# Kernel optimization log

Hardware: AMD Instinct MI355X
Metric: run time of the kernel (lower is better)

The kernel has to match this reference:

```python
import jax, jax.numpy as jnp
import numpy as np

TOP_K = 2000
NUM_DETS = 1000
BASE_LAYER_RANGE = (24.0, 48.0, 24.0, 48.0)  # (min_y, max_y, min_x, max_x) from db.configs


def _topk(heat, K):
    # heat: [B, C, H, W] -> topk over flattened C*H*W (CornerNet-style)
    B, C, H, W = heat.shape
    scores, inds = jax.lax.top_k(heat.reshape(B, -1), K)
    clses = inds // (H * W)
    sp_inds = inds % (H * W)            # spatial index into H*W
    ys = (sp_inds // W).astype(heat.dtype)
    xs = (sp_inds % W).astype(heat.dtype)
    return scores, sp_inds, clses, ys, xs


def _transpose_and_gather(feat, ind):
    # feat: [B, C, H, W], ind: [B, K] spatial indices -> [B, K, C]
    B, C, H, W = feat.shape
    feat = feat.transpose(0, 2, 3, 1).reshape(B, H * W, C)
    return feat[jnp.arange(B)[:, None], ind]


def _gather_feat(feat, ind):
    # feat: [B, N, C], ind: [B, K] -> [B, K, C]
    B = feat.shape[0]
    return feat[jnp.arange(B)[:, None], ind]


def _decode_layer(heat, tl_regr, br_regr, H0, W0, layer_idx):
    B, C, H, W = heat.shape
    dt = heat.dtype
    height_scale = 8.0 * H0 / H
    width_scale = 8.0 * W0 / W
    K = min(TOP_K, H * W)
    scores, inds, clses, ys, xs = _topk(heat, K)
    ys = ys.reshape(B, K, 1)
    xs = xs.reshape(B, K, 1)
    tlr = _transpose_and_gather(tl_regr, inds).reshape(B, K, 1, 2)
    brr = _transpose_and_gather(br_regr, inds).reshape(B, K, 1, 2)
    min_y, max_y, min_x, max_x = [v / 8.0 / 2.0 for v in BASE_LAYER_RANGE]
    tl_xs = xs - ((max_x - min_x) * tlr[..., 0] + (max_x + min_x) / 2.0)
    tl_ys = ys - ((max_y - min_y) * tlr[..., 1] + (max_y + min_y) / 2.0)
    br_xs = xs + ((max_x - min_x) * brr[..., 0] + (max_x + min_x) / 2.0)
    br_ys = ys + ((max_y - min_y) * brr[..., 1] + (max_y + min_y) / 2.0)
    bboxes = jnp.stack((tl_xs, tl_ys, br_xs, br_ys), axis=3)  # [B, K, 1, 4]
    sc = scores.reshape(B, K, 1)
    invalid = (br_xs < tl_xs) | (br_ys < tl_ys)
    sc = jnp.where(invalid, jnp.asarray(-1.0, dt), sc)
    sc = sc.reshape(B, -1)
    nd = min(NUM_DETS, sc.shape[1])
    sc, top = jax.lax.top_k(sc, nd)
    sc = sc[:, :, None]
    bboxes = _gather_feat(bboxes.reshape(B, -1, 4), top)
    bboxes = bboxes * jnp.asarray([width_scale, height_scale, width_scale, height_scale], dt)
    # layer_detections: zeros [B, nd, 7]; [:,:,:5] = cat([scores, bboxes]); then row 6 set to i
    det = jnp.concatenate([sc, bboxes, jnp.zeros((B, nd, 2), dt)], axis=2)
    det = det.at[:, 6, :].set(jnp.asarray(float(layer_idx), dt))  # faithful to `[:, 6] = i`
    return det


def setup_inputs() -> dict:
    key = jax.random.key(0)
    ks = jax.random.split(key, 9)
    B, C = 16, 80
    sizes = [(128, 128), (64, 64), (32, 32)]
    inp = {}
    for i, (H, W) in enumerate(sizes):
        inp[f"heat{i}"] = jax.random.uniform(ks[3 * i], (B, C, H, W), dtype=jnp.float32)
        inp[f"tl{i}"] = jax.random.normal(ks[3 * i + 1], (B, 2, H, W), dtype=jnp.float32)
        inp[f"br{i}"] = jax.random.normal(ks[3 * i + 2], (B, 2, H, W), dtype=jnp.float32)
    return inp


def reference(heat0, heat1, heat2, tl0, tl1, tl2, br0, br1, br2):
    heats = [heat0, heat1, heat2]
    tls = [tl0, tl1, tl2]
    brs = [br0, br1, br2]
    _, _, H0, W0 = heats[0].shape
    dets = [_decode_layer(heats[i], tls[i], brs[i], H0, W0, i) for i in range(3)]
    detections = jnp.concatenate(dets, axis=1)  # [B, sum_nd, 7]
    nd = min(NUM_DETS, detections.shape[1])
    _, top = jax.lax.top_k(detections[:, :, 0], nd)
    return _gather_feat(detections, top)
```

## Files before the change

### kernel.cpp

```cpp
#include <hip/hip_runtime.h>


#define NB 1024
#define CAP2 2048
#define CHUNK_H 32768
#define CHUNK_C 16384
#define LCAP 1024

__device__ __forceinline__ unsigned int ord_f32(float f) {
    unsigned int b = __float_as_uint(f);
    return (b & 0x80000000u) ? ~b : (b | 0x80000000u);
}
__device__ __forceinline__ float unord_f32(unsigned int o) {
    unsigned int b = (o & 0x80000000u) ? (o & 0x7fffffffu) : ~o;
    return __uint_as_float(b);
}
__device__ __forceinline__ int bucket_of(float f) {
    int bi = (int)(f * (float)NB);
    bi = bi < 0 ? 0 : (bi > NB - 1 ? NB - 1 : bi);
    return bi;
}

__device__ __forceinline__ int layer_N(int l)  { return (l == 0) ? 1310720 : (l == 1) ? 327680 : 81920; }
__device__ __forceinline__ int hist_nchunks(int l) { return (l == 0) ? 40 : (l == 1) ? 10 : 3; }
__device__ __forceinline__ int hist_base(int l)    { return (l == 0) ? 0 : (l == 1) ? 640 : 800; }

__global__ __launch_bounds__(256) void hist_kernel(
    const float* __restrict__ h0, const float* __restrict__ h1, const float* __restrict__ h2,
    int* __restrict__ ph)
{
    int l = blockIdx.z, b = blockIdx.y, chunk = blockIdx.x;
    int nc = hist_nchunks(l);
    if (chunk >= nc) return;
    int N = layer_N(l);
    int elems = min(CHUNK_H, N - chunk * CHUNK_H);
    const float* heat = (l == 0) ? h0 : (l == 1) ? h1 : h2;
    __shared__ int lh[NB];
    for (int i = threadIdx.x; i < NB; i += 256) lh[i] = 0;
    __syncthreads();
    const float4* p = (const float4*)(heat + (size_t)b * N + (size_t)chunk * CHUNK_H);
    int n4 = elems >> 2;
    for (int i = threadIdx.x; i < n4; i += 256) {
        float4 v = p[i];
        atomicAdd(&lh[bucket_of(v.x)], 1);
        atomicAdd(&lh[bucket_of(v.y)], 1);
        atomicAdd(&lh[bucket_of(v.z)], 1);
        atomicAdd(&lh[bucket_of(v.w)], 1);
    }
    __syncthreads();
    int pidx = hist_base(l) + b * nc + chunk;
    int* dst = ph + (size_t)pidx * NB;
    for (int i = threadIdx.x; i < NB; i += 256) dst[i] = lh[i];
}

__global__ __launch_bounds__(256) void thresh_kernel(const int* __restrict__ ph,
                                                     int* __restrict__ tb,
                                                     int* __restrict__ cnt)
{
    int b = blockIdx.x & 15;
    int l = blockIdx.x >> 4;
    int bl = l * 16 + b;
    if (threadIdx.x < 2) cnt[bl * 2 + threadIdx.x] = 0;
    int K = (l == 2) ? 1024 : 2000;
    int nc = hist_nchunks(l);
    const int* base = ph + (size_t)(hist_base(l) + b * nc) * NB;
    __shared__ int hh[NB];
    __shared__ int seg[256];
    int s4 = 0;
    for (int j = 0; j < 4; j++) {
        int bkt = threadIdx.x * 4 + j;
        int s = 0;
        for (int c = 0; c < nc; c++) s += base[(size_t)c * NB + bkt];
        hh[bkt] = s;
        s4 += s;
    }
    seg[threadIdx.x] = s4;
    __syncthreads();
    if (threadIdx.x == 0) {
        int acc = 0, si;
        for (si = 255; si >= 0; si--) {
            if (acc + seg[si] >= K) break;
            acc += seg[si];
        }
        if (si < 0) si = 0;
        int bidx = si * 4 + 3;
        for (; bidx > si * 4; bidx--) {
            acc += hh[bidx];
            if (acc >= K) break;
        }
        tb[bl] = bidx;
    }
}

__global__ __launch_bounds__(256) void collect_kernel(
    const float* __restrict__ h0, const float* __restrict__ h1, const float* __restrict__ h2,
    const int* __restrict__ tb, int* __restrict__ cnt, unsigned long long* __restrict__ cand)
{
    int l = blockIdx.z, b = blockIdx.y, chunk = blockIdx.x;
    int N = layer_N(l);
    if (chunk * CHUNK_C >= N) return;
    const float* heat = (l == 0) ? h0 : (l == 1) ? h1 : h2;
    int t = tb[l * 16 + b];
    int bl = l * 16 + b;

    __shared__ int lc[2];
    __shared__ int gb[2];
    __shared__ unsigned long long lbuf[2][LCAP];
    if (threadIdx.x < 2) lc[threadIdx.x] = 0;
    __syncthreads();

    const float4* p = (const float4*)(heat + (size_t)b * N + (size_t)chunk * CHUNK_C);
    int base = chunk * CHUNK_C;
    for (int i = threadIdx.x; i < CHUNK_C / 4; i += 256) {
        float4 v = p[i];
        float vs[4] = {v.x, v.y, v.z, v.w};
#pragma unroll
        for (int cc = 0; cc < 4; cc++) {
            int bk = bucket_of(vs[cc]);
            if (bk >= t) {
                int which = (bk > t) ? 0 : 1;
                int pos = atomicAdd(&lc[which], 1);
                if (pos < LCAP) {
                    unsigned int idx = (unsigned int)(base + 4 * i + cc);
                    lbuf[which][pos] = ((unsigned long long)ord_f32(vs[cc]) << 32) | (unsigned int)(~idx);
                }
            }
        }
    }
    __syncthreads();
    if (threadIdx.x < 2) {
        int n = min(lc[threadIdx.x], LCAP);
        gb[threadIdx.x] = atomicAdd(cnt + bl * 2 + threadIdx.x, n);
    }
    __syncthreads();
#pragma unroll
    for (int w = 0; w < 2; w++) {
        int n = min(lc[w], LCAP);
        unsigned long long* cd = cand + ((size_t)bl * 2 + w) * CAP2;
        int g0 = gb[w];
        for (int i = threadIdx.x; i < n; i += 256) {
            int pos = g0 + i;
            if (pos < CAP2) cd[pos] = lbuf[w][i];
        }
    }
}


__device__ __forceinline__ unsigned long long shfl_xor_u64(unsigned long long a, int j) {
    unsigned int lo = (unsigned int)a, hi = (unsigned int)(a >> 32);
    lo = (unsigned int)__shfl_xor((int)lo, j, 64);
    hi = (unsigned int)__shfl_xor((int)hi, j, 64);
    return ((unsigned long long)hi << 32) | lo;
}

template<int K, int J>
struct PhaseH {
    static __device__ __forceinline__ void run(unsigned long long (&v)[8], int base, int lane) {
        constexpr int JR = J >> 6;
#pragma unroll
        for (int r = 0; r < 8; r++) {
            if ((r & JR) == 0) {
                int i = base | (r << 6) | lane;
                unsigned long long a = v[r], bb = v[r | JR];
                bool sw = ((i & K) == 0) ? (a < bb) : (a > bb);
                if (sw) { v[r] = bb; v[r | JR] = a; }
            }
        }
        PhaseH<K, (J >> 1)>::run(v, base, lane);
    }
};

template<int K>
struct PhaseH<K, 32> {
    static __device__ __forceinline__ void run(unsigned long long (&v)[8], int base, int lane) {
#pragma unroll
        for (int js = 32; js >= 1; js >>= 1) {
            if (K > js) {
#pragma unroll
                for (int r = 0; r < 8; r++) {
                    unsigned long long a = v[r];
                    unsigned long long w = shfl_xor_u64(a, js);
                    int i = base | (r << 6) | lane;
                    bool upper = (lane & js) != 0;
                    bool keep_max = (((i & K) == 0) != upper);
                    bool agw = a > w;
                    v[r] = (keep_max == agw) ? a : w;
                }
            }
        }
    }
};

template<int K>
struct StageH {
    static __device__ __forceinline__ void run(unsigned long long (&v)[8], int base, int lane) {
        PhaseH<K, (K > 64 ? (K >> 1) : 32)>::run(v, base, lane);
        StageH<(K << 1)>::run(v, base, lane);
    }
};
template<>
struct StageH<1024> {
    static __device__ __forceinline__ void run(unsigned long long (&)[8], int, int) {}
};

template<int K, int J>
__device__ __forceinline__ void lds_exchange(unsigned long long (&v)[8],
                                             unsigned long long* lds, int base, int lane) {
    __syncthreads();
#pragma unroll
    for (int r = 0; r < 8; r++) lds[base | (r << 6) | lane] = v[r];
    __syncthreads();
#pragma unroll
    for (int r = 0; r < 8; r++) {
        int i = base | (r << 6) | lane;
        unsigned long long w = lds[i ^ J];
        bool upper = (i & J) != 0;
        bool keep_max = (((i & K) == 0) != upper);
        bool agw = v[r] > w;
        v[r] = (keep_max == agw) ? v[r] : w;
    }
}

__global__ __launch_bounds__(256) void sort_kernel(const int* __restrict__ cnt,
                                                   unsigned long long* __restrict__ cand)
{
    int idx = blockIdx.x;
    int n = min(cnt[idx], CAP2);
    unsigned long long* src = cand + (size_t)idx * CAP2;
    __shared__ unsigned long long lds[CAP2];
    int tid = threadIdx.x;
    int lane = tid & 63;
    int base = (tid >> 6) << 9;

    unsigned long long v[8];
#pragma unroll
    for (int r = 0; r < 8; r++) {
        int i = base | (r << 6) | lane;
        v[r] = (i < n) ? src[i] : 0ull;
    }

    StageH<2>::run(v, base, lane);

    lds_exchange<1024, 512>(v, lds, base, lane);
    PhaseH<1024, 256>::run(v, base, lane);

    lds_exchange<2048, 1024>(v, lds, base, lane);
    lds_exchange<2048, 512>(v, lds, base, lane);
    PhaseH<2048, 256>::run(v, base, lane);

#pragma unroll
    for (int r = 0; r < 8; r++) src[base | (r << 6) | lane] = v[r];
}

__global__ __launch_bounds__(1024) void build_kernel(
    const float* __restrict__ t0, const float* __restrict__ t1, const float* __restrict__ t2,
    const float* __restrict__ r0, const float* __restrict__ r1, const float* __restrict__ r2,
    const int* __restrict__ cnt, const unsigned long long* __restrict__ cand,
    float* __restrict__ det)
{
    int l = blockIdx.x >> 4;
    int b = blockIdx.x & 15;
    int bl = l * 16 + b;
    int HW = (l == 0) ? 16384 : (l == 1) ? 4096 : 1024;
    int W  = (l == 0) ? 128 : (l == 1) ? 64 : 32;
    int K  = (l == 2) ? 1024 : 2000;
    float scale = (l == 0) ? 8.f : (l == 1) ? 16.f : 32.f;
    const float* tlp = (l == 0) ? t0 : (l == 1) ? t1 : t2;
    const float* brp = (l == 0) ? r0 : (l == 1) ? r1 : r2;

    int n_hi = min(cnt[bl * 2], CAP2);
    const unsigned long long* hi = cand + (size_t)(bl * 2) * CAP2;
    const unsigned long long* bd = cand + (size_t)(bl * 2 + 1) * CAP2;

    __shared__ int wsum[16];
    int tid = threadIdx.x;
    int lane = tid & 63, wid = tid >> 6;

    float s_[2], bx_[2][4];
    int f_[2];
#pragma unroll
    for (int q = 0; q < 2; q++) {
        int k = 2 * tid + q;
        f_[q] = 0;
        if (k < K) {
            unsigned long long kk = (k < n_hi) ? hi[k] : bd[k - n_hi];
            unsigned int idx = ~(unsigned int)kk;
            float score = unord_f32((unsigned int)(kk >> 32));
            int sp = (int)(idx % (unsigned)HW);
            float xs = (float)(sp % W), ys = (float)(sp / W);
            float tv0 = tlp[((size_t)b * 2 + 0) * HW + sp];
            float tv1 = tlp[((size_t)b * 2 + 1) * HW + sp];
            float bv0 = brp[((size_t)b * 2 + 0) * HW + sp];
            float bv1 = brp[((size_t)b * 2 + 1) * HW + sp];
            float tlx = __fsub_rn(xs, __fadd_rn(__fmul_rn(1.5f, tv0), 2.25f));
            float tly = __fsub_rn(ys, __fadd_rn(__fmul_rn(1.5f, tv1), 2.25f));
            float brx = __fadd_rn(xs, __fadd_rn(__fmul_rn(1.5f, bv0), 2.25f));
            float bry = __fadd_rn(ys, __fadd_rn(__fmul_rn(1.5f, bv1), 2.25f));
            bool invalid = (brx < tlx) || (bry < tly);
            f_[q] = invalid ? 0 : 1;
            s_[q] = invalid ? -1.0f : score;
            bx_[q][0] = __fmul_rn(tlx, scale);
            bx_[q][1] = __fmul_rn(tly, scale);
            bx_[q][2] = __fmul_rn(brx, scale);
            bx_[q][3] = __fmul_rn(bry, scale);
        }
    }
    int mysum = f_[0] + f_[1];

    int x = mysum;
#pragma unroll
    for (int off = 1; off < 64; off <<= 1) {
        int y = __shfl_up(x, off, 64);
        if (lane >= off) x += y;
    }
    if (lane == 63) wsum[wid] = x;
    __syncthreads();
    if (wid == 0 && lane < 16) {
        int s = wsum[lane];
#pragma unroll
        for (int off = 1; off < 16; off <<= 1) {
            int y = __shfl_up(s, off, 64);
            if (lane >= off) s += y;
        }
        wsum[lane] = s;
    }
    __syncthreads();
    int wave_off = (wid > 0) ? wsum[wid - 1] : 0;
    int V = wsum[15];
    int base_excl = (x + wave_off) - mysum;

    float* dbase = det + ((size_t)b * 3000 + (size_t)l * 1000) * 7;
#pragma unroll
    for (int q = 0; q < 2; q++) {
        int k = 2 * tid + q;
        if (k < K) {
            int pos = base_excl + (q == 1 ? f_[0] : 0);
            int rank = f_[q] ? pos : V + (k - pos);
            if (rank < 1000 && rank != 6) {
                float* drow = dbase + (size_t)rank * 7;
                drow[0] = s_[q];
                drow[1] = bx_[q][0];
                drow[2] = bx_[q][1];
                drow[3] = bx_[q][2];
                drow[4] = bx_[q][3];
                drow[5] = 0.f;
                drow[6] = 0.f;
            }
        }
    }
    if (tid == 0) {
        float lv = (float)l;
        float* drow = dbase + 6 * 7;
#pragma unroll
        for (int j = 0; j < 7; j++) drow[j] = lv;
    }
}

__device__ __forceinline__ bool key_gt(float sa, int ga, float sb, int gb) {
    return (sa > sb) || (sa == sb && ga < gb);
}

__global__ __launch_bounds__(1024) void final_kernel(const float* __restrict__ det,
                                                     float* __restrict__ out)
{
    int b = blockIdx.x;
    __shared__ float sc[3000];
    int tid = threadIdx.x;
    const float* dbase = det + (size_t)b * 3000 * 7;
    for (int i = tid; i < 3000; i += 1024) sc[i] = dbase[(size_t)i * 7];
    __syncthreads();

    for (int e = tid; e < 3000; e += 1024) {
        float se = sc[e];
        int ge = e;
        int rank = 0;
#pragma unroll
        for (int lp = 0; lp < 3; lp++) {
            int lo = 0, hiB = 999;
            while (lo < hiB) {
                int mid = (lo + hiB) >> 1;
                int p = mid + (mid >= 6 ? 1 : 0);
                int g = lp * 1000 + p;
                if (key_gt(sc[g], g, se, ge)) lo = mid + 1; else hiB = mid;
            }
            rank += lo;
        }
#pragma unroll
        for (int ls = 0; ls < 3; ls++) {
            int g = ls * 1000 + 6;
            if (g != e && key_gt((float)ls, g, se, ge)) rank++;
        }
        if (rank < 1000) {
            const float* src = dbase + (size_t)e * 7;
            float* dst = out + ((size_t)b * 1000 + rank) * 7;
#pragma unroll
            for (int j = 0; j < 7; j++) dst[j] = src[j];
        }
    }
}

extern "C" void kernel_launch(void* const* d_in, const int* in_sizes, int n_in,
                              void* d_out, int out_size, void* d_ws, size_t ws_size,
                              hipStream_t stream)
{
    (void)in_sizes; (void)n_in; (void)out_size; (void)ws_size;
    const float* h0 = (const float*)d_in[0];
    const float* t0 = (const float*)d_in[1];
    const float* r0 = (const float*)d_in[2];
    const float* h1 = (const float*)d_in[3];
    const float* t1 = (const float*)d_in[4];
    const float* r1 = (const float*)d_in[5];
    const float* h2 = (const float*)d_in[6];
    const float* t2 = (const float*)d_in[7];
    const float* r2 = (const float*)d_in[8];
    float* out = (float*)d_out;

    char* ws = (char*)d_ws;
    int* ph   = (int*)ws;
    int* cnt  = (int*)(ws + 3473408);
    int* tb   = (int*)(ws + 3473792);
    unsigned long long* cand = (unsigned long long*)(ws + 3473984);
    float* det = (float*)(ws + 5046848);

    hist_kernel<<<dim3(40, 16, 3), 256, 0, stream>>>(h0, h1, h2, ph);
    thresh_kernel<<<48, 256, 0, stream>>>(ph, tb, cnt);
    collect_kernel<<<dim3(80, 16, 3), 256, 0, stream>>>(h0, h1, h2, tb, cnt, cand);
    sort_kernel<<<96, 256, 0, stream>>>(cnt, cand);
    build_kernel<<<48, 1024, 0, stream>>>(t0, t1, t2, r0, r1, r2, cnt, cand, det);
    final_kernel<<<16, 1024, 0, stream>>>(det, out);
}
```

Baseline: 256.8 us.

## Fuse histogram and candidate collection with fixed loose threshold to avoid second heat pass

The histogram pass now also collects candidates above a fixed per-layer loose bucket threshold into per-chunk global buffers, and the threshold kernel filters those loose candidates directly, so the separate collect kernel that re-read every heatmap is gone. If the computed threshold falls below the loose threshold or a chunk overflows, a single block rescans the whole heatmap as a fallback. This removes one full read of roughly 110 MB of heat data and a launch, but adds atomics and shared-memory buffering to the histogram kernel. The fallback path would be very slow because one block per batch-layer scans millions of elements.

New measurement: 255.7 us. No clear change (-0.4%).

```diff
diff --git a/kernel.cpp b/kernel.cpp
--- a/kernel.cpp
+++ b/kernel.cpp
@@ -3,9 +3,7 @@
 
 #define NB 1024
 #define CAP2 2048
-#define CHUNK_H 32768
-#define CHUNK_C 16384
-#define LCAP 1024
+#define CHUNK 32768
 
 __device__ __forceinline__ unsigned int ord_f32(float f) {
     unsigned int b = __float_as_uint(f);
@@ -22,61 +20,95 @@
 }
 
 __device__ __forceinline__ int layer_N(int l)  { return (l == 0) ? 1310720 : (l == 1) ? 327680 : 81920; }
-__device__ __forceinline__ int hist_nchunks(int l) { return (l == 0) ? 40 : (l == 1) ? 10 : 3; }
-__device__ __forceinline__ int hist_base(int l)    { return (l == 0) ? 0 : (l == 1) ? 640 : 800; }
-
-__global__ __launch_bounds__(256) void hist_kernel(
+__device__ __forceinline__ int nchunks(int l)  { return (l == 0) ? 40 : (l == 1) ? 10 : 3; }
+__device__ __forceinline__ int hist_base(int l){ return (l == 0) ? 0 : (l == 1) ? 640 : 800; }
+__device__ __forceinline__ int TL_of(int l)    { return (l == 0) ? NB - 4 : (l == 1) ? NB - 16 : NB - 32; }
+__device__ __forceinline__ int bl_cap(int l)   { return (l == 0) ? 512 : (l == 1) ? 1024 : 2048; }
+__device__ __forceinline__ int loose_base(int l){ return (l == 0) ? 0 : (l == 1) ? 327680 : 491520; }
+
+__global__ __launch_bounds__(256) void fused_kernel(
     const float* __restrict__ h0, const float* __restrict__ h1, const float* __restrict__ h2,
-    int* __restrict__ ph)
+    int* __restrict__ ph, int* __restrict__ pbc, unsigned long long* __restrict__ loose)
 {
     int l = blockIdx.z, b = blockIdx.y, chunk = blockIdx.x;
-    int nc = hist_nchunks(l);
+    int nc = nchunks(l);
     if (chunk >= nc) return;
     int N = layer_N(l);
-    int elems = min(CHUNK_H, N - chunk * CHUNK_H);
+    int elems = min(CHUNK, N - chunk * CHUNK);
     const float* heat = (l == 0) ? h0 : (l == 1) ? h1 : h2;
+    int TL = TL_of(l);
+
     __shared__ int lh[NB];
+    __shared__ int lc;
+    __shared__ unsigned long long lbuf[2048];
     for (int i = threadIdx.x; i < NB; i += 256) lh[i] = 0;
-    __syncthreads();
-    const float4* p = (const float4*)(heat + (size_t)b * N + (size_t)chunk * CHUNK_H);
+    if (threadIdx.x == 0) lc = 0;
+    __syncthreads();
+
+    const float4* p = (const float4*)(heat + (size_t)b * N + (size_t)chunk * CHUNK);
+    int base = chunk * CHUNK;
     int n4 = elems >> 2;
     for (int i = threadIdx.x; i < n4; i += 256) {
         float4 v = p[i];
-        atomicAdd(&lh[bucket_of(v.x)], 1);
-        atomicAdd(&lh[bucket_of(v.y)], 1);
-        atomicAdd(&lh[bucket_of(v.z)], 1);
-        atomicAdd(&lh[bucket_of(v.w)], 1);
+        float vs[4] = {v.x, v.y, v.z, v.w};
+#pragma unroll
+        for (int cc = 0; cc < 4; cc++) {
+            int bk = bucket_of(vs[cc]);
+            atomicAdd(&lh[bk], 1);
+            if (bk >= TL) {
+                int pos = atomicAdd(&lc, 1);
+                if (pos < 2048) {
+                    unsigned int idx = (unsigned int)(base + 4 * i + cc);
+                    lbuf[pos] = ((unsigned long long)ord_f32(vs[cc]) << 32) | (unsigned int)(~idx);
+                }
+            }
+        }
     }
     __syncthreads();
     int pidx = hist_base(l) + b * nc + chunk;
     int* dst = ph + (size_t)pidx * NB;
     for (int i = threadIdx.x; i < NB; i += 256) dst[i] = lh[i];
-}
-
-__global__ __launch_bounds__(256) void thresh_kernel(const int* __restrict__ ph,
-                                                     int* __restrict__ tb,
-                                                     int* __restrict__ cnt)
+    if (threadIdx.x == 0) pbc[pidx] = lc;
+    int cap = bl_cap(l);
+    int n = min(lc, min(cap, 2048));
+    unsigned long long* seg = loose + loose_base(l) + (size_t)(b * nc + chunk) * cap;
+    for (int i = threadIdx.x; i < n; i += 256) seg[i] = lbuf[i];
+}
+
+__global__ __launch_bounds__(256) void partition_kernel(
+    const float* __restrict__ h0, const float* __restrict__ h1, const float* __restrict__ h2,
+    const int* __restrict__ ph, const int* __restrict__ pbc,
+    const unsigned long long* __restrict__ loose,
+    int* __restrict__ cnt, unsigned long long* __restrict__ cand)
 {
     int b = blockIdx.x & 15;
     int l = blockIdx.x >> 4;
     int bl = l * 16 + b;
-    if (threadIdx.x < 2) cnt[bl * 2 + threadIdx.x] = 0;
     int K = (l == 2) ? 1024 : 2000;
-    int nc = hist_nchunks(l);
-    const int* base = ph + (size_t)(hist_base(l) + b * nc) * NB;
+    int nc = nchunks(l);
+    int cap = bl_cap(l);
+    const int* hbase = ph + (size_t)(hist_base(l) + b * nc) * NB;
+
     __shared__ int hh[NB];
     __shared__ int seg[256];
+    __shared__ int st;
+    __shared__ int repf;
+    __shared__ int lc[2];
+    __shared__ unsigned long long lbuf[2][2048];
+    int tid = threadIdx.x;
+
     int s4 = 0;
     for (int j = 0; j < 4; j++) {
-        int bkt = threadIdx.x * 4 + j;
+        int bkt = tid * 4 + j;
         int s = 0;
-        for (int c = 0; c < nc; c++) s += base[(size_t)c * NB + bkt];
+        for (int c = 0; c < nc; c++) s += hbase[(size_t)c * NB + bkt];
         hh[bkt] = s;
         s4 += s;
     }
-    seg[threadIdx.x] = s4;
-    __syncthreads();
-    if (threadIdx.x == 0) {
+    seg[tid] = s4;
+    if (tid == 0) { repf = 0; lc[0] = 0; lc[1] = 0; }
+    __syncthreads();
+    if (tid == 0) {
         int acc = 0, si;
         for (si = 255; si >= 0; si--) {
             if (acc + seg[si] >= K) break;
@@ -88,60 +120,58 @@
             acc += hh[bidx];
             if (acc >= K) break;
         }
-        tb[bl] = bidx;
-    }
-}
-
-__global__ __launch_bounds__(256) void collect_kernel(
-    const float* __restrict__ h0, const float* __restrict__ h1, const float* __restrict__ h2,
-    const int* __restrict__ tb, int* __restrict__ cnt, unsigned long long* __restrict__ cand)
-{
-    int l = blockIdx.z, b = blockIdx.y, chunk = blockIdx.x;
-    int N = layer_N(l);
-    if (chunk * CHUNK_C >= N) return;
-    const float* heat = (l == 0) ? h0 : (l == 1) ? h1 : h2;
-    int t = tb[l * 16 + b];
-    int bl = l * 16 + b;
-
-    __shared__ int lc[2];
-    __shared__ int gb[2];
-    __shared__ unsigned long long lbuf[2][LCAP];
-    if (threadIdx.x < 2) lc[threadIdx.x] = 0;
-    __syncthreads();
-
-    const float4* p = (const float4*)(heat + (size_t)b * N + (size_t)chunk * CHUNK_C);
-    int base = chunk * CHUNK_C;
-    for (int i = threadIdx.x; i < CHUNK_C / 4; i += 256) {
-        float4 v = p[i];
-        float vs[4] = {v.x, v.y, v.z, v.w};
-#pragma unroll
-        for (int cc = 0; cc < 4; cc++) {
-            int bk = bucket_of(vs[cc]);
-            if (bk >= t) {
-                int which = (bk > t) ? 0 : 1;
-                int pos = atomicAdd(&lc[which], 1);
-                if (pos < LCAP) {
-                    unsigned int idx = (unsigned int)(base + 4 * i + cc);
-                    lbuf[which][pos] = ((unsigned long long)ord_f32(vs[cc]) << 32) | (unsigned int)(~idx);
+        st = bidx;
+        if (bidx < TL_of(l)) repf = 1;
+    }
+    __syncthreads();
+    int t = st;
+    for (int c = tid; c < nc; c += 256)
+        if (pbc[hist_base(l) + b * nc + c] > min(cap, 2048)) repf = 1;
+    __syncthreads();
+
+    if (!repf) {
+        const unsigned long long* lb = loose + loose_base(l) + (size_t)b * nc * cap;
+        for (int c = 0; c < nc; c++) {
+            int n_c = min(pbc[hist_base(l) + b * nc + c], min(cap, 2048));
+            const unsigned long long* sg = lb + (size_t)c * cap;
+            for (int i = tid; i < n_c; i += 256) {
+                unsigned long long key = sg[i];
+                int bk = bucket_of(unord_f32((unsigned int)(key >> 32)));
+                if (bk >= t) {
+                    int which = (bk > t) ? 0 : 1;
+                    int pos = atomicAdd(&lc[which], 1);
+                    if (pos < 2048) lbuf[which][pos] = key;
                 }
             }
         }
-    }
-    __syncthreads();
-    if (threadIdx.x < 2) {
-        int n = min(lc[threadIdx.x], LCAP);
-        gb[threadIdx.x] = atomicAdd(cnt + bl * 2 + threadIdx.x, n);
+    } else {
+        int N = layer_N(l);
+        const float* heat = (l == 0) ? h0 : (l == 1) ? h1 : h2;
+        const float4* p = (const float4*)(heat + (size_t)b * N);
+        for (int i = tid; i < (N >> 2); i += 256) {
+            float4 v = p[i];
+            float vs[4] = {v.x, v.y, v.z, v.w};
+#pragma unroll
+            for (int cc = 0; cc < 4; cc++) {
+                int bk = bucket_of(vs[cc]);
+                if (bk >= t) {
+                    int which = (bk > t) ? 0 : 1;
+                    int pos = atomicAdd(&lc[which], 1);
+                    if (pos < 2048) {
+                        unsigned int idx = (unsigned int)(4 * i + cc);
+                        lbuf[which][pos] = ((unsigned long long)ord_f32(vs[cc]) << 32) | (unsigned int)(~idx);
+                    }
+                }
+            }
+        }
     }
     __syncthreads();
 #pragma unroll
     for (int w = 0; w < 2; w++) {
-        int n = min(lc[w], LCAP);
+        int n = min(lc[w], CAP2);
+        if (tid == 0) cnt[bl * 2 + w] = n;
         unsigned long long* cd = cand + ((size_t)bl * 2 + w) * CAP2;
-        int g0 = gb[w];
-        for (int i = threadIdx.x; i < n; i += 256) {
-            int pos = g0 + i;
-            if (pos < CAP2) cd[pos] = lbuf[w][i];
-        }
+        for (int i = tid; i < n; i += 256) cd[i] = lbuf[w][i];
     }
 }
 
@@ -417,14 +447,14 @@
 
     char* ws = (char*)d_ws;
     int* ph   = (int*)ws;
-    int* cnt  = (int*)(ws + 3473408);
-    int* tb   = (int*)(ws + 3473792);
-    unsigned long long* cand = (unsigned long long*)(ws + 3473984);
-    float* det = (float*)(ws + 5046848);
-
-    hist_kernel<<<dim3(40, 16, 3), 256, 0, stream>>>(h0, h1, h2, ph);
-    thresh_kernel<<<48, 256, 0, stream>>>(ph, tb, cnt);
-    collect_kernel<<<dim3(80, 16, 3), 256, 0, stream>>>(h0, h1, h2, tb, cnt, cand);
+    int* pbc  = (int*)(ws + 3473408);
+    unsigned long long* loose = (unsigned long long*)(ws + 3476800);
+    int* cnt  = (int*)(ws + 8195392);
+    unsigned long long* cand  = (unsigned long long*)(ws + 8195776);
+    float* det = (float*)(ws + 9768640);
+
+    fused_kernel<<<dim3(40, 16, 3), 256, 0, stream>>>(h0, h1, h2, ph, pbc, loose);
+    partition_kernel<<<48, 256, 0, stream>>>(h0, h1, h2, ph, pbc, loose, cnt, cand);
     sort_kernel<<<96, 256, 0, stream>>>(cnt, cand);
     build_kernel<<<48, 1024, 0, stream>>>(t0, t1, t2, r0, r1, r2, cnt, cand, det);
     final_kernel<<<16, 1024, 0, stream>>>(det, out);
```
